# Kernel optimization log

Measured on AMD Instinct MI355X. Metric: run time of the kernel, lower is better.

## Reference

```python
import jax, jax.numpy as jnp
import numpy as np

NUM_NODES = 50000
NUM_EDGES = 1600000
IN_C = 512
OUT_C = 512


def setup_inputs() -> dict:
    key = jax.random.key(0)
    k1, k2, k3, k4 = jax.random.split(key, 4)
    x = jax.random.normal(k1, (NUM_NODES, IN_C), dtype=jnp.float32)
    edge_index = jax.random.randint(k2, (2, NUM_EDGES), 0, NUM_NODES, dtype=jnp.int64)
    # nn.Linear params (kaiming-uniform-ish scale)
    lim = 1.0 / np.sqrt(IN_C)
    W = jax.random.uniform(k3, (OUT_C, IN_C), dtype=jnp.float32, minval=-lim, maxval=lim)
    b = jax.random.uniform(k4, (OUT_C,), dtype=jnp.float32, minval=-lim, maxval=lim)
    return {"x": x, "edge_index": edge_index, "W": W, "b": b}


def reference(x, edge_index, W, b):
    num_nodes = x.shape[0]
    src = edge_index[0]
    tar = edge_index[1]
    # dense layer: feat = x @ W^T + b  -> [N, out_c]
    feat = jnp.einsum('ni,oi->no', x, W) + b
    # degree: scatter_add of ones over src, plus self-loop term (+1)
    ones_e = jnp.ones((src.shape[0],), dtype=feat.dtype)
    deg = jax.ops.segment_sum(ones_e, src, num_segments=num_nodes) + 1.0
    deg_inv_sqrt = jnp.where(deg > 0, deg ** -0.5, 0.0)
    # per-edge normalized weight
    w = deg_inv_sqrt[src] * deg_inv_sqrt[tar]  # [E]
    # sparse-coo matmul: out[src] += w * feat[tar]
    msgs = w[:, None] * feat[tar]  # [E, out_c]
    out = jax.ops.segment_sum(msgs, src, num_segments=num_nodes)
    # self contribution: feat * deg^{-1}
    out = out + feat * (1.0 / deg)[:, None]
    return out
```

## Files before the change

kernel.cpp:

```cpp
#include <hip/hip_runtime.h>

#define IN_C 512
#define OUT_C 512

typedef __attribute__((ext_vector_type(4))) float f32x4;
typedef __attribute__((ext_vector_type(8))) short bf16x8;

__device__ __forceinline__ unsigned short f2bf_rne(float f) {
    unsigned int u = __float_as_uint(f);
    u += 0x7fffu + ((u >> 16) & 1u);
    return (unsigned short)(u >> 16);
}
__device__ __forceinline__ float bflo(unsigned int u) { return __uint_as_float(u << 16); }
__device__ __forceinline__ float bfhi(unsigned int u) { return __uint_as_float(u & 0xffff0000u); }

__global__ void k_convert(const float* __restrict__ in, unsigned short* __restrict__ out, int n8) {
    int i = blockIdx.x * blockDim.x + threadIdx.x;
    if (i >= n8) return;
    const float4* in4 = (const float4*)in;
    float4 a = in4[i * 2], b = in4[i * 2 + 1];
    uint4 o;
    o.x = (unsigned)f2bf_rne(a.x) | ((unsigned)f2bf_rne(a.y) << 16);
    o.y = (unsigned)f2bf_rne(a.z) | ((unsigned)f2bf_rne(a.w) << 16);
    o.z = (unsigned)f2bf_rne(b.x) | ((unsigned)f2bf_rne(b.y) << 16);
    o.w = (unsigned)f2bf_rne(b.z) | ((unsigned)f2bf_rne(b.w) << 16);
    *(uint4*)&out[(size_t)i * 8] = o;
}

__global__ void k_degree(const int* __restrict__ src, int E, int* __restrict__ deg) {
    int e = blockIdx.x * blockDim.x + threadIdx.x;
    if (e < E) atomicAdd(&deg[src[e]], 1);
}

__global__ void k_dinv(const int* __restrict__ deg, int N, float* __restrict__ dinv) {
    int n = blockIdx.x * blockDim.x + threadIdx.x;
    if (n < N) dinv[n] = rsqrtf((float)(deg[n] + 1));
}

__global__ void k_scan(const int* __restrict__ deg, int N, int* __restrict__ row_start) {
    __shared__ int wsum[16];
    int t = threadIdx.x;
    int wave = t >> 6, lane = t & 63;
    int carry = 0;
    int nChunks = (N + 1023) >> 10;
    for (int c = 0; c < nChunks; ++c) {
        int i = (c << 10) + t;
        int v = (i < N) ? deg[i] : 0;
        int s = v;
#pragma unroll
        for (int off = 1; off < 64; off <<= 1) {
            int u = __shfl_up(s, off, 64);
            if (lane >= off) s += u;
        }
        if (lane == 63) wsum[wave] = s;
        __syncthreads();
        if (wave == 0 && lane < 16) {
            int ws = wsum[lane];
#pragma unroll
            for (int off = 1; off < 16; off <<= 1) {
                int u = __shfl_up(ws, off, 64);
                if (lane >= off) ws += u;
            }
            wsum[lane] = ws;
        }
        __syncthreads();
        int waveOff = (wave == 0) ? 0 : wsum[wave - 1];
        if (i < N) row_start[i] = s - v + waveOff + carry;
        int total = wsum[15];
        __syncthreads();
        carry += total;
    }
    if (t == 0) row_start[N] = carry;
}

__global__ void k_fill(const int* __restrict__ src, const int* __restrict__ tar, int E,
                       const int* __restrict__ row_start, int* __restrict__ fill,
                       int* __restrict__ csr_tar) {
    int e = blockIdx.x * blockDim.x + threadIdx.x;
    if (e < E) {
        int s = src[e];
        int p = atomicAdd(&fill[s], 1);
        csr_tar[row_start[s] + p] = tar[e];
    }
}

__global__ __launch_bounds__(256) void k_gemm_mfma(const unsigned short* __restrict__ xb,
                                                   const unsigned short* __restrict__ wb,
                                                   const float* __restrict__ bias,
                                                   unsigned short* __restrict__ featb, int N) {
    int tid = threadIdx.x;
    int wave = tid >> 6, lane = tid & 63;
    int wr = wave >> 1, wc = wave & 1;
    int rowBase = blockIdx.y * 128 + wr * 64;
    int colBase = blockIdx.x * 128 + wc * 64;
    int r0 = lane & 15;
    int kg = lane >> 4;

    f32x4 acc[4][4];
#pragma unroll
    for (int mi = 0; mi < 4; ++mi)
#pragma unroll
        for (int ni = 0; ni < 4; ++ni)
            acc[mi][ni] = (f32x4){0.f, 0.f, 0.f, 0.f};

    for (int k0 = 0; k0 < IN_C; k0 += 32) {
        bf16x8 a[4], b[4];
#pragma unroll
        for (int mi = 0; mi < 4; ++mi) {
            int r = rowBase + mi * 16 + r0;
            if (r > N - 1) r = N - 1;
            a[mi] = *(const bf16x8*)&xb[(size_t)r * IN_C + k0 + kg * 8];
        }
#pragma unroll
        for (int ni = 0; ni < 4; ++ni) {
            int ccol = colBase + ni * 16 + r0;
            b[ni] = *(const bf16x8*)&wb[(size_t)ccol * IN_C + k0 + kg * 8];
        }
#pragma unroll
        for (int mi = 0; mi < 4; ++mi)
#pragma unroll
            for (int ni = 0; ni < 4; ++ni)
                acc[mi][ni] = __builtin_amdgcn_mfma_f32_16x16x32_bf16(a[mi], b[ni], acc[mi][ni], 0, 0, 0);
    }

    float bv[4];
#pragma unroll
    for (int ni = 0; ni < 4; ++ni) bv[ni] = bias[colBase + ni * 16 + r0];

#pragma unroll
    for (int mi = 0; mi < 4; ++mi) {
#pragma unroll
        for (int reg = 0; reg < 4; ++reg) {
            int grow = rowBase + mi * 16 + kg * 4 + reg;
            if (grow < N) {
#pragma unroll
                for (int ni = 0; ni < 4; ++ni) {
                    float v = acc[mi][ni][reg] + bv[ni];
                    featb[(size_t)grow * OUT_C + colBase + ni * 16 + r0] = f2bf_rne(v);
                }
            }
        }
    }
}

__global__ __launch_bounds__(256) void k_aggregate(const unsigned short* __restrict__ featb,
                                                   const float* __restrict__ dinv,
                                                   const int* __restrict__ row_start,
                                                   const int* __restrict__ csr_tar,
                                                   float* __restrict__ out, int N) {
    int wave = threadIdx.x >> 6, lane = threadIdx.x & 63;
    int n = blockIdx.x * 4 + wave;
    if (n >= N) return;
    float din = dinv[n];
    int rs = row_start[n], re = row_start[n + 1];
    float accf[8] = {0.f, 0.f, 0.f, 0.f, 0.f, 0.f, 0.f, 0.f};

    for (int base = rs; base < re; base += 64) {
        int m = re - base;
        if (m > 64) m = 64;
        int t_l = 0;
        float w_l = 0.f;
        if (lane < m) {
            t_l = csr_tar[base + lane];
            w_l = din * dinv[t_l];
        }
        for (int j = 0; j < m; ++j) {
            int t = __shfl(t_l, j, 64);
            float w = __shfl(w_l, j, 64);
            uint4 v = *(const uint4*)&featb[(size_t)t * OUT_C + lane * 8];
            accf[0] += w * bflo(v.x);
            accf[1] += w * bfhi(v.x);
            accf[2] += w * bflo(v.y);
            accf[3] += w * bfhi(v.y);
            accf[4] += w * bflo(v.z);
            accf[5] += w * bfhi(v.z);
            accf[6] += w * bflo(v.w);
            accf[7] += w * bfhi(v.w);
        }
    }

    {
        uint4 v = *(const uint4*)&featb[(size_t)n * OUT_C + lane * 8];
        float sw = din * din;
        accf[0] += sw * bflo(v.x);
        accf[1] += sw * bfhi(v.x);
        accf[2] += sw * bflo(v.y);
        accf[3] += sw * bfhi(v.y);
        accf[4] += sw * bflo(v.z);
        accf[5] += sw * bfhi(v.z);
        accf[6] += sw * bflo(v.w);
        accf[7] += sw * bfhi(v.w);
    }
    float4 o0 = {accf[0], accf[1], accf[2], accf[3]};
    float4 o1 = {accf[4], accf[5], accf[6], accf[7]};
    *(float4*)&out[(size_t)n * OUT_C + lane * 8] = o0;
    *(float4*)&out[(size_t)n * OUT_C + lane * 8 + 4] = o1;
}

extern "C" void kernel_launch(void* const* d_in, const int* in_sizes, int n_in,
                              void* d_out, int out_size, void* d_ws, size_t ws_size,
                              hipStream_t stream) {
    const float* x    = (const float*)d_in[0];
    const int*   ei   = (const int*)d_in[1];
    const float* W    = (const float*)d_in[2];
    const float* bias = (const float*)d_in[3];
    float* out = (float*)d_out;

    int N = in_sizes[0] / IN_C;
    int E = in_sizes[1] / 2;
    const int* src = ei;
    const int* tar = ei + E;

    char* ws = (char*)d_ws;
    unsigned short* featb = (unsigned short*)ws;
    size_t off = (size_t)N * OUT_C * sizeof(unsigned short);
    unsigned short* xb = (unsigned short*)(ws + off);
    size_t xb_off = off;
    off += (size_t)N * IN_C * sizeof(unsigned short);
    unsigned short* wb = (unsigned short*)(ws + off);
    off += (size_t)OUT_C * IN_C * sizeof(unsigned short);
    float* dinv = (float*)(ws + off);      off += (size_t)N * sizeof(float);
    int* deg = (int*)(ws + off);           off += (size_t)N * sizeof(int);
    int* fill = (int*)(ws + off);          off += (size_t)N * sizeof(int);
    int* row_start = (int*)(ws + off);     off += (size_t)(N + 1) * sizeof(int);
    int* csr_tar = (int*)(ws + xb_off);

    int n8x = N * IN_C / 8;
    k_convert<<<(n8x + 255) / 256, 256, 0, stream>>>(x, xb, n8x);
    int n8w = OUT_C * IN_C / 8;
    k_convert<<<(n8w + 255) / 256, 256, 0, stream>>>(W, wb, n8w);
    dim3 g(OUT_C / 128, (N + 127) / 128);
    k_gemm_mfma<<<g, 256, 0, stream>>>(xb, wb, bias, featb, N);

    hipMemsetAsync(deg, 0, 2 * (size_t)N * sizeof(int), stream);
    k_degree<<<(E + 255) / 256, 256, 0, stream>>>(src, E, deg);
    k_dinv<<<(N + 255) / 256, 256, 0, stream>>>(deg, N, dinv);
    k_scan<<<1, 1024, 0, stream>>>(deg, N, row_start);
    k_fill<<<(E + 255) / 256, 256, 0, stream>>>(src, tar, E, row_start, fill, csr_tar);

    k_aggregate<<<(N + 3) / 4, 256, 0, stream>>>(featb, dinv, row_start, csr_tar, out, N);
}
```

Measured before the change: 716.2 us.

## Parallelize CSR prefix scan across blocks and unroll aggregation gathers by four

Replaces the single-block serial prefix scan over node degrees with a three-kernel multi-block scan (per-block scan, block-sum scan, add-back), and folds the dinv computation into the first scan kernel. The aggregation loop now issues four independent feature-row gathers per iteration to expose more memory-level parallelism. Adds two small kernel launches, and the block-sum scan assumes at most 64 blocks, which limits N to 65536.

```diff
diff --git a/kernel.cpp b/kernel.cpp
--- a/kernel.cpp
+++ b/kernel.cpp
@@ -32,45 +32,56 @@
     if (e < E) atomicAdd(&deg[src[e]], 1);
 }
 
-__global__ void k_dinv(const int* __restrict__ deg, int N, float* __restrict__ dinv) {
-    int n = blockIdx.x * blockDim.x + threadIdx.x;
-    if (n < N) dinv[n] = rsqrtf((float)(deg[n] + 1));
-}
-
-__global__ void k_scan(const int* __restrict__ deg, int N, int* __restrict__ row_start) {
+__global__ __launch_bounds__(1024) void k_scan1(const int* __restrict__ deg, int N,
+                                                int* __restrict__ row_start,
+                                                int* __restrict__ bsum,
+                                                float* __restrict__ dinv) {
     __shared__ int wsum[16];
     int t = threadIdx.x;
     int wave = t >> 6, lane = t & 63;
-    int carry = 0;
-    int nChunks = (N + 1023) >> 10;
-    for (int c = 0; c < nChunks; ++c) {
-        int i = (c << 10) + t;
-        int v = (i < N) ? deg[i] : 0;
-        int s = v;
-#pragma unroll
-        for (int off = 1; off < 64; off <<= 1) {
-            int u = __shfl_up(s, off, 64);
-            if (lane >= off) s += u;
-        }
-        if (lane == 63) wsum[wave] = s;
-        __syncthreads();
-        if (wave == 0 && lane < 16) {
-            int ws = wsum[lane];
-#pragma unroll
-            for (int off = 1; off < 16; off <<= 1) {
-                int u = __shfl_up(ws, off, 64);
-                if (lane >= off) ws += u;
-            }
-            wsum[lane] = ws;
-        }
-        __syncthreads();
-        int waveOff = (wave == 0) ? 0 : wsum[wave - 1];
-        if (i < N) row_start[i] = s - v + waveOff + carry;
-        int total = wsum[15];
-        __syncthreads();
-        carry += total;
-    }
-    if (t == 0) row_start[N] = carry;
+    int i = blockIdx.x * 1024 + t;
+    int v = (i < N) ? deg[i] : 0;
+    if (i < N) dinv[i] = rsqrtf((float)(v + 1));
+    int s = v;
+#pragma unroll
+    for (int off = 1; off < 64; off <<= 1) {
+        int u = __shfl_up(s, off, 64);
+        if (lane >= off) s += u;
+    }
+    if (lane == 63) wsum[wave] = s;
+    __syncthreads();
+    if (wave == 0 && lane < 16) {
+        int ws = wsum[lane];
+#pragma unroll
+        for (int off = 1; off < 16; off <<= 1) {
+            int u = __shfl_up(ws, off, 64);
+            if (lane >= off) ws += u;
+        }
+        wsum[lane] = ws;
+    }
+    __syncthreads();
+    int waveOff = (wave == 0) ? 0 : wsum[wave - 1];
+    if (i < N) row_start[i] = s - v + waveOff;
+    if (t == 0) bsum[blockIdx.x] = wsum[15];
+}
+
+__global__ void k_scan2(int* __restrict__ bsum, int nb) {
+    int lane = threadIdx.x & 63;
+    int v = (lane < nb) ? bsum[lane] : 0;
+    int s = v;
+#pragma unroll
+    for (int off = 1; off < 64; off <<= 1) {
+        int u = __shfl_up(s, off, 64);
+        if (lane >= off) s += u;
+    }
+    if (lane < nb) bsum[lane] = s - v;
+    if (lane == 63) bsum[nb] = s;
+}
+
+__global__ void k_scan3(int* __restrict__ row_start, const int* __restrict__ bsum, int N, int nb) {
+    int i = blockIdx.x * blockDim.x + threadIdx.x;
+    if (i < N) row_start[i] += bsum[i >> 10];
+    if (i == 0) row_start[N] = bsum[nb];
 }
 
 __global__ void k_fill(const int* __restrict__ src, const int* __restrict__ tar, int E,
@@ -143,6 +154,13 @@
     }
 }
 
+__device__ __forceinline__ void acc8(float* accf, uint4 v, float wgt) {
+    accf[0] += wgt * bflo(v.x); accf[1] += wgt * bfhi(v.x);
+    accf[2] += wgt * bflo(v.y); accf[3] += wgt * bfhi(v.y);
+    accf[4] += wgt * bflo(v.z); accf[5] += wgt * bfhi(v.z);
+    accf[6] += wgt * bflo(v.w); accf[7] += wgt * bfhi(v.w);
+}
+
 __global__ __launch_bounds__(256) void k_aggregate(const unsigned short* __restrict__ featb,
                                                    const float* __restrict__ dinv,
                                                    const int* __restrict__ row_start,
@@ -164,32 +182,32 @@
             t_l = csr_tar[base + lane];
             w_l = din * dinv[t_l];
         }
-        for (int j = 0; j < m; ++j) {
+        int j = 0;
+        for (; j + 4 <= m; j += 4) {
+            int t0 = __shfl(t_l, j, 64),     t1 = __shfl(t_l, j + 1, 64);
+            int t2 = __shfl(t_l, j + 2, 64), t3 = __shfl(t_l, j + 3, 64);
+            float w0 = __shfl(w_l, j, 64),     w1 = __shfl(w_l, j + 1, 64);
+            float w2 = __shfl(w_l, j + 2, 64), w3 = __shfl(w_l, j + 3, 64);
+            uint4 v0 = *(const uint4*)&featb[(size_t)t0 * OUT_C + lane * 8];
+            uint4 v1 = *(const uint4*)&featb[(size_t)t1 * OUT_C + lane * 8];
+            uint4 v2 = *(const uint4*)&featb[(size_t)t2 * OUT_C + lane * 8];
+            uint4 v3 = *(const uint4*)&featb[(size_t)t3 * OUT_C + lane * 8];
+            acc8(accf, v0, w0);
+            acc8(accf, v1, w1);
+            acc8(accf, v2, w2);
+            acc8(accf, v3, w3);
+        }
+        for (; j < m; ++j) {
             int t = __shfl(t_l, j, 64);
             float w = __shfl(w_l, j, 64);
             uint4 v = *(const uint4*)&featb[(size_t)t * OUT_C + lane * 8];
-            accf[0] += w * bflo(v.x);
-            accf[1] += w * bfhi(v.x);
-            accf[2] += w * bflo(v.y);
-            accf[3] += w * bfhi(v.y);
-            accf[4] += w * bflo(v.z);
-            accf[5] += w * bfhi(v.z);
-            accf[6] += w * bflo(v.w);
-            accf[7] += w * bfhi(v.w);
+            acc8(accf, v, w);
         }
     }
 
     {
         uint4 v = *(const uint4*)&featb[(size_t)n * OUT_C + lane * 8];
-        float sw = din * din;
-        accf[0] += sw * bflo(v.x);
-        accf[1] += sw * bfhi(v.x);
-        accf[2] += sw * bflo(v.y);
-        accf[3] += sw * bfhi(v.y);
-        accf[4] += sw * bflo(v.z);
-        accf[5] += sw * bfhi(v.z);
-        accf[6] += sw * bflo(v.w);
-        accf[7] += sw * bfhi(v.w);
+        acc8(accf, v, din * din);
     }
     float4 o0 = {accf[0], accf[1], accf[2], accf[3]};
     float4 o1 = {accf[4], accf[5], accf[6], accf[7]};
@@ -210,6 +228,7 @@
     int E = in_sizes[1] / 2;
     const int* src = ei;
     const int* tar = ei + E;
+    int nb = (N + 1023) >> 10;
 
     char* ws = (char*)d_ws;
     unsigned short* featb = (unsigned short*)ws;
@@ -223,6 +242,7 @@
     int* deg = (int*)(ws + off);           off += (size_t)N * sizeof(int);
     int* fill = (int*)(ws + off);          off += (size_t)N * sizeof(int);
     int* row_start = (int*)(ws + off);     off += (size_t)(N + 1) * sizeof(int);
+    int* bsum = (int*)(ws + off);          off += (size_t)(nb + 1) * sizeof(int);
     int* csr_tar = (int*)(ws + xb_off);
 
     int n8x = N * IN_C / 8;
@@ -232,10 +252,11 @@
     dim3 g(OUT_C / 128, (N + 127) / 128);
     k_gemm_mfma<<<g, 256, 0, stream>>>(xb, wb, bias, featb, N);
 
-    hipMemsetAsync(deg, 0, 2 * (size_t)N * sizeof(int), stream);
+    (void)hipMemsetAsync(deg, 0, 2 * (size_t)N * sizeof(int), stream);
     k_degree<<<(E + 255) / 256, 256, 0, stream>>>(src, E, deg);
-    k_dinv<<<(N + 255) / 256, 256, 0, stream>>>(deg, N, dinv);
-    k_scan<<<1, 1024, 0, stream>>>(deg, N, row_start);
+    k_scan1<<<nb, 1024, 0, stream>>>(deg, N, row_start, bsum, dinv);
+    k_scan2<<<1, 64, 0, stream>>>(bsum, nb);
+    k_scan3<<<(N + 255) / 256, 256, 0, stream>>>(row_start, bsum, N, nb);
     k_fill<<<(E + 255) / 256, 256, 0, stream>>>(src, tar, E, row_start, fill, csr_tar);
 
     k_aggregate<<<(N + 3) / 4, 256, 0, stream>>>(featb, dinv, row_start, csr_tar, out, N);
```

After: 681.1 us. -4.9%, faster.
